# Performance work log

Hardware: AMD Instinct MI355X
Metric: run time of the kernel (lower is better)

Reference implementation:

```python
import jax, jax.numpy as jnp
import numpy as np

B, N_C, N_T = 8, 2048, 2048
D_S, D_F = 2, 1
K = 32
EMB_OBS = 4
H = 64
N_RBF = 16
NUM_BLKS = 6
RBF_GAMMA = 10.0


def _layer_norm(x, g, b):
    m = jnp.mean(x, -1, keepdims=True)
    v = jnp.var(x, -1, keepdims=True)
    return (x - m) * jax.lax.rsqrt(v + 1e-6) * g + b


def setup_inputs() -> dict:
    key = jax.random.key(0)
    ks = jax.random.split(key, 16)
    D_IN = EMB_OBS + D_S + D_F  # obs-flag embed + coords + features = 7
    return {
        "s_ctx": jax.random.normal(ks[0], (B, N_C, D_S)),
        "f_ctx": jax.random.normal(ks[1], (B, N_C, D_F)),
        "s_test": jax.random.normal(ks[2], (B, N_T, D_S)),
        "obs_table": jax.random.normal(ks[3], (2, EMB_OBS)) * 0.1,
        "emb_w0": jax.random.normal(ks[4], (D_IN, 256)) / np.sqrt(D_IN),
        "emb_b0": jnp.zeros((256,)),
        "emb_w1": jax.random.normal(ks[5], (256, 128)) / np.sqrt(256.0),
        "emb_b1": jnp.zeros((128,)),
        "emb_w2": jax.random.normal(ks[6], (128, H)) / np.sqrt(128.0),
        "emb_b2": jnp.zeros((H,)),
        "ln_g": jnp.ones((H,)),
        "ln_b": jnp.zeros((H,)),
        "rbf_centers": jnp.tile(jnp.linspace(0.0, 4.0, N_RBF)[None, :], (NUM_BLKS, 1)),
        "rbf_w": jax.random.normal(ks[7], (NUM_BLKS, N_RBF)) / np.sqrt(N_RBF),
        "rbf_b": jnp.zeros((NUM_BLKS,)),
        "blk_w1": jax.random.normal(ks[8], (NUM_BLKS, 2 * H, 2 * H)) / np.sqrt(2.0 * H),
        "blk_b1": jnp.zeros((NUM_BLKS, 2 * H)),
        "blk_w2": jax.random.normal(ks[9], (NUM_BLKS, 2 * H, H)) / np.sqrt(2.0 * H),
        "blk_b2": jnp.zeros((NUM_BLKS, H)),
        "blk_ln_g": jnp.ones((NUM_BLKS, H)),
        "blk_ln_b": jnp.zeros((NUM_BLKS, H)),
        "head_w0": jax.random.normal(ks[10], (H, 256)) / np.sqrt(float(H)),
        "head_b0": jnp.zeros((256,)),
        "head_w1": jax.random.normal(ks[11], (256, 64)) / np.sqrt(256.0),
        "head_b1": jnp.zeros((64,)),
        "head_w2": jax.random.normal(ks[12], (64, 2)) / np.sqrt(64.0),
        "head_b2": jnp.zeros((2,)),
    }


def reference(s_ctx, f_ctx, s_test, obs_table, emb_w0, emb_b0, emb_w1, emb_b1,
              emb_w2, emb_b2, ln_g, ln_b, rbf_centers, rbf_w, rbf_b,
              blk_w1, blk_b1, blk_w2, blk_b2, blk_ln_g, blk_ln_b,
              head_w0, head_b0, head_w1, head_b1, head_w2, head_b2):
    Bq, N_c = s_ctx.shape[:2]
    N_t = s_test.shape[1]

    # --- embed: obs flag + coords + (zeroed for test) function values ---
    obs_c = jnp.broadcast_to(obs_table[1], (Bq, N_c, EMB_OBS))  # observed = 1
    obs_t = jnp.broadcast_to(obs_table[0], (Bq, N_t, EMB_OBS))  # unobserved = 0
    f_test = jnp.zeros((Bq, N_t, f_ctx.shape[-1]), f_ctx.dtype)
    ctx = jnp.concatenate([obs_c, s_ctx, f_ctx], -1)
    test = jnp.concatenate([obs_t, s_test, f_test], -1)

    def emb(x):
        h = jax.nn.gelu(x @ emb_w0 + emb_b0)
        h = jax.nn.gelu(h @ emb_w1 + emb_b1)
        return h @ emb_w2 + emb_b2

    x_ctx = _layer_norm(emb(ctx), ln_g, ln_b)
    x_test = _layer_norm(emb(test), ln_g, ln_b)

    # --- kNN graph build (queries -> context senders) ---
    def knn(q, s):
        d2 = jnp.sum((q[:, :, None, :] - s[:, None, :, :]) ** 2, -1)  # (B, Nq, Nc)
        neg, idx = jax.lax.top_k(-d2, K)
        return idx, jnp.sqrt(jnp.maximum(-neg, 1e-12))

    idx_cc, d_cc = knn(s_ctx, s_ctx)
    idx_ct, d_ct = knn(s_test, s_ctx)
    off = (jnp.arange(Bq) * N_c)[:, None, None]
    senders = jnp.concatenate([(idx_cc + off).reshape(-1), (idx_ct + off).reshape(-1)])
    edges = jnp.concatenate([d_cc.reshape(-1), d_ct.reshape(-1)])
    nodes = jnp.concatenate([x_ctx.reshape(Bq * N_c, H), x_test.reshape(Bq * N_t, H)], 0)
    n_node = Bq * (N_c + N_t)
    # receivers = repeat(arange(n_node), K): each node owns a contiguous K-edge block
    send2d = senders.reshape(n_node, K)
    e2d = edges.reshape(n_node, K)
    mask2d = jnp.isfinite(e2d)
    e_safe = jnp.where(mask2d, e2d, 0.0)

    # --- RBF-biased message-passing blocks ---
    for l in range(NUM_BLKS):
        feats = jnp.exp(-RBF_GAMMA * (e_safe[..., None] - rbf_centers[l]) ** 2)  # (n_node, K, N_RBF)
        bias = feats @ rbf_w[l] + rbf_b[l]                                       # (n_node, K)
        bias = jnp.where(mask2d, bias, -1e9)
        w = jax.nn.softmax(bias, axis=-1)
        agg = jnp.einsum('nk,nkh->nh', w, nodes[send2d])  # gather senders + weighted sum
        h = jnp.concatenate([nodes, agg], -1)
        h = jax.nn.gelu(h @ blk_w1[l] + blk_b1[l])
        h = h @ blk_w2[l] + blk_b2[l]
        nodes = _layer_norm(nodes + h, blk_ln_g[l], blk_ln_b[l])

    # --- head + diagonal MVN ---
    x_t = nodes[-Bq * N_t:].reshape(Bq, N_t, H)
    h = jax.nn.gelu(x_t @ head_w0 + head_b0)
    h = jax.nn.gelu(h @ head_w1 + head_b1)
    out = h @ head_w2 + head_b2
    mean = out[..., 0]
    std = jax.nn.softplus(out[..., 1]) + 1e-3
    return mean, std
```

## Files before the change

kernel.cpp:

```cpp
#include <hip/hip_runtime.h>
#include <hip/hip_bf16.h>
#include <hip/hip_fp16.h>
#include <math.h>

using bf16 = __hip_bfloat16;

#define N_CTX   2048
#define N_TST   2048
#define NB      8
#define KNN     32
#define HDIM    64
#define NRBF    16
#define N_CTX_NODES (NB * N_CTX)
#define N_NODE      (NB * (N_CTX + N_TST))
#define POOL_CAP 256

typedef __attribute__((ext_vector_type(8))) short short8;
typedef __attribute__((ext_vector_type(4))) float f32x4;

#define SWZ(r, k) ((k) ^ (((r) & 7) << 3))

__device__ __forceinline__ bool is_f32(const void* probe) {
    return ((const unsigned short*)probe)[0] == 0;
}
__device__ __forceinline__ float ld(const void* p, int i, bool f32) {
    return f32 ? ((const float*)p)[i]
               : __bfloat162float(((const bf16*)p)[i]);
}
__device__ __forceinline__ unsigned short f2b(float x) {
    bf16 h = __float2bfloat16(x); unsigned short u;
    __builtin_memcpy(&u, &h, 2); return u;
}
__device__ __forceinline__ float b2f(unsigned short u) {
    bf16 h; __builtin_memcpy(&h, &u, 2); return __bfloat162float(h);
}
__device__ __forceinline__ unsigned short f2h(float x) {
    __half h = __float2half(x); unsigned short u;
    __builtin_memcpy(&u, &h, 2); return u;
}
__device__ __forceinline__ float h2f(unsigned short u) {
    __half h; __builtin_memcpy(&h, &u, 2); return __half2float(h);
}
__device__ __forceinline__ float gelu_tanh(float x) {
    float u = -1.5957691216057308f * (x + 0.044715f * x * x * x);
    return x * __builtin_amdgcn_rcpf(1.0f + __expf(u));
}
__device__ __forceinline__ unsigned long long shfl_u64(unsigned long long v, int src) {
    int lo = __shfl((int)(unsigned)v, src);
    int hi = __shfl((int)(unsigned)(v >> 32), src);
    return ((unsigned long long)(unsigned)hi << 32) | (unsigned)lo;
}

__device__ __forceinline__ void batch_barrier(unsigned* cnt, unsigned target) {
    __syncthreads();
    if (threadIdx.x == 0) {
        __hip_atomic_fetch_add(cnt, 1u, __ATOMIC_RELEASE, __HIP_MEMORY_SCOPE_AGENT);
        unsigned v;
        do {
            v = __hip_atomic_load(cnt, __ATOMIC_ACQUIRE, __HIP_MEMORY_SCOPE_AGENT);
            if (v < target) __builtin_amdgcn_s_sleep(2);
        } while (v < target);
    }
    __syncthreads();
}

__global__ __launch_bounds__(512)
void embed_kernel(const void* s_ctx, const void* f_ctx, const void* s_test,
                  const void* obs, const void* w0, const void* b0,
                  const void* w1, const void* b1, const void* w2, const void* b2,
                  const void* ln_g, const void* ln_b,
                  unsigned short* __restrict__ ctxb, float* __restrict__ testf) {
    bool f32 = is_f32(ln_g);
    int tid = threadIdx.x, w = tid >> 6, l = tid & 63;
    int nb = blockIdx.x * 64;
    bool is_test = (nb >= N_CTX_NODES);
    int loc0 = is_test ? nb - N_CTX_NODES : nb;
    int b = loc0 >> 11;

    __shared__ unsigned short A[64 * 128];
    __shared__ unsigned short W[256 * 128];
    __shared__ unsigned short H0[64 * 256];
    __shared__ unsigned short W2[64 * 128];

    for (int idx = tid; idx < 64 * 128; idx += 512) A[idx] = 0;
    for (int idx = tid; idx < 256 * 128; idx += 512) W[idx] = 0;
    __syncthreads();

    {
        int nn = tid >> 3, slot = tid & 7;
        if (slot < 7) {
            int loc = loc0 + nn;
            int i = loc & (N_CTX - 1);
            float v;
            if (slot < 4)       v = ld(obs, (is_test ? 0 : 1) * 4 + slot, f32);
            else if (slot < 6)  v = is_test ? ld(s_test, (b * N_TST + i) * 2 + slot - 4, f32)
                                            : ld(s_ctx,  (b * N_CTX + i) * 2 + slot - 4, f32);
            else                v = is_test ? 0.0f : ld(f_ctx, b * N_CTX + i, f32);
            A[nn * 128 + SWZ(nn, slot)] = f2b(v);
        }
    }
    for (int idx = tid; idx < 7 * 256; idx += 512) {
        int k = idx >> 8, c = idx & 255;
        W[c * 128 + SWZ(c, k)] = f2b(ld(w0, idx, f32));
    }
    __syncthreads();

    {
        int rt = w & 3, co = w >> 2;
        int ra = rt * 16 + (l & 15);
        int kb = (l >> 4) << 3;
        short8 av = *(const short8*)&A[ra * 128 + SWZ(ra, kb)];
        f32x4 acc[8];
        #pragma unroll
        for (int c8 = 0; c8 < 8; ++c8) acc[c8] = (f32x4){0.f, 0.f, 0.f, 0.f};
        #pragma unroll
        for (int c8 = 0; c8 < 8; ++c8) {
            int cb = co * 8 + c8;
            int rb = cb * 16 + (l & 15);
            short8 bv = *(const short8*)&W[rb * 128 + SWZ(rb, kb)];
            acc[c8] = __builtin_amdgcn_mfma_f32_16x16x32_bf16(av, bv, acc[c8], 0, 0, 0);
        }
        #pragma unroll
        for (int c8 = 0; c8 < 8; ++c8) {
            int col = (co * 8 + c8) * 16 + (l & 15);
            float bb = ld(b0, col, f32);
            #pragma unroll
            for (int reg = 0; reg < 4; ++reg) {
                int r = rt * 16 + (l >> 4) * 4 + reg;
                H0[r * 256 + SWZ(r, col)] = f2b(gelu_tanh(acc[c8][reg] + bb));
            }
        }
    }
    __syncthreads();

    for (int idx = tid; idx < 256 * 128; idx += 512) {
        int k = idx >> 7, c = idx & 127;
        W[c * 256 + SWZ(c, k)] = f2b(ld(w1, idx, f32));
    }
    for (int idx = tid; idx < 128 * 64; idx += 512) {
        int k = idx >> 6, c = idx & 63;
        W2[c * 128 + SWZ(c, k)] = f2b(ld(w2, idx, f32));
    }
    __syncthreads();

    {
        int rt = w & 3, cq = w >> 2;
        int ra = rt * 16 + (l & 15);
        f32x4 acc[4];
        #pragma unroll
        for (int c4 = 0; c4 < 4; ++c4) acc[c4] = (f32x4){0.f, 0.f, 0.f, 0.f};
        #pragma unroll
        for (int ks = 0; ks < 8; ++ks) {
            int kb = ks * 32 + ((l >> 4) << 3);
            short8 av = *(const short8*)&H0[ra * 256 + SWZ(ra, kb)];
            #pragma unroll
            for (int c4 = 0; c4 < 4; ++c4) {
                int cb = cq * 4 + c4;
                int rb = cb * 16 + (l & 15);
                short8 bv = *(const short8*)&W[rb * 256 + SWZ(rb, kb)];
                acc[c4] = __builtin_amdgcn_mfma_f32_16x16x32_bf16(av, bv, acc[c4], 0, 0, 0);
            }
        }
        #pragma unroll
        for (int c4 = 0; c4 < 4; ++c4) {
            int col = (cq * 4 + c4) * 16 + (l & 15);
            float bb = ld(b1, col, f32);
            #pragma unroll
            for (int reg = 0; reg < 4; ++reg) {
                int r = rt * 16 + (l >> 4) * 4 + reg;
                A[r * 128 + SWZ(r, col)] = f2b(gelu_tanh(acc[c4][reg] + bb));
            }
        }
    }
    __syncthreads();

    if (w < 4) {
        f32x4 a2[4];
        #pragma unroll
        for (int cb = 0; cb < 4; ++cb) a2[cb] = (f32x4){0.f, 0.f, 0.f, 0.f};
        int ra = w * 16 + (l & 15);
        #pragma unroll
        for (int ks = 0; ks < 4; ++ks) {
            int kb = ks * 32 + ((l >> 4) << 3);
            short8 av = *(const short8*)&A[ra * 128 + SWZ(ra, kb)];
            #pragma unroll
            for (int cb = 0; cb < 4; ++cb) {
                int rb = cb * 16 + (l & 15);
                short8 bv = *(const short8*)&W2[rb * 128 + SWZ(rb, kb)];
                a2[cb] = __builtin_amdgcn_mfma_f32_16x16x32_bf16(av, bv, a2[cb], 0, 0, 0);
            }
        }
        int colb = l & 15;
        float g4[4], bb4[4], b24[4];
        #pragma unroll
        for (int cb = 0; cb < 4; ++cb) {
            int col = cb * 16 + colb;
            g4[cb]  = ld(ln_g, col, f32);
            bb4[cb] = ld(ln_b, col, f32);
            b24[cb] = ld(b2,  col, f32);
        }
        #pragma unroll
        for (int reg = 0; reg < 4; ++reg) {
            int r = w * 16 + (l >> 4) * 4 + reg;
            float vv[4]; float s = 0.f, s2 = 0.f;
            #pragma unroll
            for (int cb = 0; cb < 4; ++cb) {
                float v = a2[cb][reg] + b24[cb];
                vv[cb] = v; s += v; s2 += v * v;
            }
            #pragma unroll
            for (int o = 8; o > 0; o >>= 1) { s += __shfl_xor(s, o); s2 += __shfl_xor(s2, o); }
            float m = s / 64.0f;
            float var = s2 / 64.0f - m * m;
            float rs = rsqrtf(var + 1e-6f);
            #pragma unroll
            for (int cb = 0; cb < 4; ++cb) {
                int col = cb * 16 + colb;
                float val = (vv[cb] - m) * rs * g4[cb] + bb4[cb];
                if (is_test) testf[(loc0 + r) * HDIM + col] = val;
                else         ctxb[(size_t)(nb + r) * HDIM + col] = f2b(val);
            }
        }
    }
}

__global__ __launch_bounds__(512) void knn_kernel(const void* s_ctx, const void* s_test,
                                                  const void* probe,
                                                  unsigned short* __restrict__ knn_idx) {
    bool f32 = is_f32(probe);
    int w = threadIdx.x >> 6, l = threadIdx.x & 63;
    int n = blockIdx.x * 8 + w;
    __shared__ float cx[N_CTX], cy[N_CTX];
    __shared__ unsigned long long pool[8][POOL_CAP];
    __shared__ unsigned pcnt[8];

    bool is_test = (n >= N_CTX_NODES);
    int loc = is_test ? n - N_CTX_NODES : n;
    int b = loc >> 11, q = loc & (N_CTX - 1);

    for (int j = threadIdx.x; j < N_CTX; j += 512) {
        cx[j] = ld(s_ctx, (b * N_CTX + j) * 2 + 0, f32);
        cy[j] = ld(s_ctx, (b * N_CTX + j) * 2 + 1, f32);
    }
    __syncthreads();

    float qx = is_test ? ld(s_test, (b * N_TST + q) * 2 + 0, f32) : cx[q];
    float qy = is_test ? ld(s_test, (b * N_TST + q) * 2 + 1, f32) : cy[q];

    unsigned dbits[32];
    unsigned bmin = 0xFFFFFFFFu;
    #pragma unroll
    for (int i = 0; i < 32; ++i) {
        int j = i * 64 + l;
        float dx = qx - cx[j], dy = qy - cy[j];
        float d2 = __fadd_rn(__fmul_rn(dx, dx), __fmul_rn(dy, dy));
        unsigned ub = __float_as_uint(d2);
        dbits[i] = ub;
        bmin = min(bmin, ub);
    }

    unsigned T = 0;
    #pragma unroll
    for (int bit = 31; bit >= 0; --bit) {
        unsigned trial = T | (1u << bit);
        int c = __popcll(__ballot(bmin < trial));
        if (c < 32) T = trial;
    }

    if (l == 0) pcnt[w] = 0;
    unsigned mycnt = 0;
    #pragma unroll
    for (int i = 0; i < 32; ++i) mycnt += (dbits[i] <= T) ? 1u : 0u;
    unsigned off = atomicAdd(&pcnt[w], mycnt);
    #pragma unroll
    for (int i = 0; i < 32; ++i) {
        if (dbits[i] <= T) {
            if (off < POOL_CAP)
                pool[w][off] = ((unsigned long long)dbits[i] << 32) | (unsigned)(i * 64 + l);
            ++off;
        }
    }
    asm volatile("s_waitcnt lgkmcnt(0)" ::: "memory");
    unsigned M = pcnt[w];
    if (M > POOL_CAP) M = POOL_CAP;

    if (M <= 128) {
        unsigned long long my0 = (l < (int)M) ? pool[w][l] : ~0ull;
        unsigned long long my1 = (64 + l < (int)M) ? pool[w][64 + l] : ~0ull;
        unsigned r0 = 0, r1 = 0;
        unsigned M0 = M < 64 ? M : 64;
        for (unsigned jp = 0; jp < M0; ++jp) {
            unsigned long long v = shfl_u64(my0, (int)jp);
            r0 += (v < my0) ? 1u : 0u;
            r1 += (v < my1) ? 1u : 0u;
        }
        for (unsigned jp = 64; jp < M; ++jp) {
            unsigned long long v = shfl_u64(my1, (int)(jp - 64));
            r0 += (v < my0) ? 1u : 0u;
            r1 += (v < my1) ? 1u : 0u;
        }
        if (l < (int)M && r0 < KNN)
            knn_idx[(size_t)n * KNN + r0] = (unsigned short)(my0 & 0xFFFFu);
        if (64 + l < (int)M && r1 < KNN)
            knn_idx[(size_t)n * KNN + r1] = (unsigned short)(my1 & 0xFFFFu);
    } else {
        for (unsigned m = l; m < M; m += 64) {
            unsigned long long me = pool[w][m];
            unsigned rank = 0;
            for (unsigned jp = 0; jp < M; ++jp)
                rank += (pool[w][jp] < me) ? 1u : 0u;
            if (rank < KNN)
                knn_idx[(size_t)n * KNN + rank] = (unsigned short)(me & 0xFFFFu);
        }
    }
}

__global__ __launch_bounds__(1024, 4)
void mp_coop_kernel(unsigned short* __restrict__ ctxA, unsigned short* __restrict__ ctxB,
                    float* __restrict__ testf,
                    const unsigned short* __restrict__ kidx,
                    unsigned* __restrict__ bar,
                    const void* s_ctx, const void* s_test,
                    const void* rbf_c, const void* rbf_w, const void* rbf_b,
                    const void* w1, const void* b1, const void* w2, const void* b2,
                    const void* lng, const void* lnb) {
    bool f32 = is_f32(lng);
    int tid = threadIdx.x, w = tid >> 6, l = tid & 63;

    int batch = blockIdx.x & 7;
    int slot  = blockIdx.x >> 3;
    bool isctx = (slot < 16);
    int lslot = slot & 15;
    int seg0 = batch * N_CTX + lslot * 128;
    int n0   = (isctx ? 0 : N_CTX_NODES) + seg0;
    int bofs = batch * N_CTX;
    unsigned* cnt = bar + batch * 16;

    __shared__ float          state[128 * 64];
    __shared__ unsigned short A0[128 * 128];
    __shared__ unsigned short h1s[128 * 128];
    __shared__ unsigned short wt[128 * 128];
    __shared__ unsigned short wk_l[128 * 32];
    __shared__ unsigned short kidx_l[128 * 32];
    __shared__ unsigned short d_l[128 * 32];

    for (int idx = tid; idx < 128 * 64; idx += 1024)
        state[idx] = isctx ? b2f(ctxA[n0 * 64 + idx]) : testf[seg0 * 64 + idx];

    for (int idx = tid; idx < 4096; idx += 1024) {
        int i = idx >> 5, kk = idx & 31;
        int n = n0 + i;
        int q = lslot * 128 + i;
        float qx = isctx ? ld(s_ctx, (bofs + q) * 2 + 0, f32)
                         : ld(s_test, (batch * N_TST + q) * 2 + 0, f32);
        float qy = isctx ? ld(s_ctx, (bofs + q) * 2 + 1, f32)
                         : ld(s_test, (batch * N_TST + q) * 2 + 1, f32);
        int si = (int)kidx[(size_t)n * KNN + kk];
        kidx_l[idx] = (unsigned short)si;
        float dx = qx - ld(s_ctx, (bofs + si) * 2 + 0, f32);
        float dy = qy - ld(s_ctx, (bofs + si) * 2 + 1, f32);
        float d2 = __fadd_rn(__fmul_rn(dx, dx), __fmul_rn(dy, dy));
        d_l[idx] = f2h(sqrtf(fmaxf(d2, 1e-12f)));
    }
    __syncthreads();

    const unsigned short* cur = ctxA;
    unsigned short* nxt = ctxB;

    for (int layer = 0; layer < 6; ++layer) {
        for (int idx = tid; idx < 16384; idx += 1024) {
            int k = idx >> 7, c = idx & 127;
            wt[c * 128 + SWZ(c, k)] = f2b(ld(w1, layer * 16384 + idx, f32));
        }
        for (int p = 0; p < 4; ++p) {
            int i = p * 32 + w * 2 + (l >> 5);
            int kk = l & 31;
            float d = h2f(d_l[i * 32 + kk]);
            float bias = ld(rbf_b, layer, f32);
            #pragma unroll
            for (int j = 0; j < NRBF; ++j) {
                float c = ld(rbf_c, layer * NRBF + j, f32);
                float u = d - c;
                bias += expf(-10.0f * u * u) * ld(rbf_w, layer * NRBF + j, f32);
            }
            float m = bias;
            #pragma unroll
            for (int o = 16; o > 0; o >>= 1) m = fmaxf(m, __shfl_xor(m, o));
            float e = expf(bias - m), s = e;
            #pragma unroll
            for (int o = 16; o > 0; o >>= 1) s += __shfl_xor(s, o);
            wk_l[i * 32 + kk] = f2h(e / s);
        }
        __syncthreads();

        {
            int m = l & 31, h = l >> 5;
            for (int i = w * 8; i < w * 8 + 8; ++i) {
                A0[i * 128 + SWZ(i, l)] = f2b(state[i * 64 + l]);
                float a0 = 0.f, a1 = 0.f, c0 = 0.f, c1 = 0.f;
                #pragma unroll
                for (int k = 0; k < 16; k += 2) {
                    {
                        int kk = 2 * k + h;
                        int si = (int)kidx_l[i * 32 + kk];
                        unsigned u = *(const unsigned*)(cur + (size_t)(bofs + si) * 64 + 2 * m);
                        float wkv = h2f(wk_l[i * 32 + kk]);
                        a0 += wkv * __uint_as_float(u << 16);
                        a1 += wkv * __uint_as_float(u & 0xFFFF0000u);
                    }
                    {
                        int kk = 2 * (k + 1) + h;
                        int si = (int)kidx_l[i * 32 + kk];
                        unsigned u = *(const unsigned*)(cur + (size_t)(bofs + si) * 64 + 2 * m);
                        float wkv = h2f(wk_l[i * 32 + kk]);
                        c0 += wkv * __uint_as_float(u << 16);
                        c1 += wkv * __uint_as_float(u & 0xFFFF0000u);
                    }
                }
                a0 += c0; a1 += c1;
                a0 += __shfl_xor(a0, 32);
                a1 += __shfl_xor(a1, 32);
                if (h == 0) {
                    unsigned pk = (unsigned)f2b(a0) | ((unsigned)f2b(a1) << 16);
                    *(unsigned*)&A0[i * 128 + SWZ(i, 64 + 2 * m)] = pk;
                }
            }
        }
        __syncthreads();

        {
            f32x4 acc[4];
            #pragma unroll
            for (int c4 = 0; c4 < 4; ++c4) acc[c4] = (f32x4){0.f, 0.f, 0.f, 0.f};
            int ra = (w & 7) * 16 + (l & 15);
            #pragma unroll
            for (int ks = 0; ks < 4; ++ks) {
                int kb = ks * 32 + ((l >> 4) << 3);
                short8 av = *(const short8*)&A0[ra * 128 + SWZ(ra, kb)];
                #pragma unroll
                for (int c4 = 0; c4 < 4; ++c4) {
                    int cb = (w >> 3) * 4 + c4;
                    int rb = cb * 16 + (l & 15);
                    short8 bv = *(const short8*)&wt[rb * 128 + SWZ(rb, kb)];
                    acc[c4] = __builtin_amdgcn_mfma_f32_16x16x32_bf16(av, bv, acc[c4], 0, 0, 0);
                }
            }
            #pragma unroll
            for (int c4 = 0; c4 < 4; ++c4) {
                int col = ((w >> 3) * 4 + c4) * 16 + (l & 15);
                float bb = ld(b1, layer * 128 + col, f32);
                #pragma unroll
                for (int reg = 0; reg < 4; ++reg) {
                    int r = (w & 7) * 16 + (l >> 4) * 4 + reg;
                    h1s[r * 128 + SWZ(r, col)] = f2b(gelu_tanh(acc[c4][reg] + bb));
                }
            }
        }
        __syncthreads();
        for (int idx = tid; idx < 8192; idx += 1024) {
            int k = idx >> 6, c = idx & 63;
            wt[c * 128 + SWZ(c, k)] = f2b(ld(w2, layer * 8192 + idx, f32));
        }
        __syncthreads();

        if (w < 8) {
            f32x4 a2[4];
            #pragma unroll
            for (int cb = 0; cb < 4; ++cb) a2[cb] = (f32x4){0.f, 0.f, 0.f, 0.f};
            int ra = w * 16 + (l & 15);
            #pragma unroll
            for (int ks = 0; ks < 4; ++ks) {
                int kb = ks * 32 + ((l >> 4) << 3);
                short8 av = *(const short8*)&h1s[ra * 128 + SWZ(ra, kb)];
                #pragma unroll
                for (int cb = 0; cb < 4; ++cb) {
                    int rb = cb * 16 + (l & 15);
                    short8 bv = *(const short8*)&wt[rb * 128 + SWZ(rb, kb)];
                    a2[cb] = __builtin_amdgcn_mfma_f32_16x16x32_bf16(av, bv, a2[cb], 0, 0, 0);
                }
            }
            int colb = l & 15;
            float g4[4], bb4[4], b24[4];
            #pragma unroll
            for (int cb = 0; cb < 4; ++cb) {
                int col = cb * 16 + colb;
                g4[cb]  = ld(lng, layer * 64 + col, f32);
                bb4[cb] = ld(lnb, layer * 64 + col, f32);
                b24[cb] = ld(b2,  layer * 64 + col, f32);
            }
            #pragma unroll
            for (int reg = 0; reg < 4; ++reg) {
                int r = w * 16 + (l >> 4) * 4 + reg;
                float vv[4]; float s = 0.f, s2 = 0.f;
                #pragma unroll
                for (int cb = 0; cb < 4; ++cb) {
                    int col = cb * 16 + colb;
                    float v = a2[cb][reg] + b24[cb] + state[r * 64 + col];
                    vv[cb] = v; s += v; s2 += v * v;
                }
                #pragma unroll
                for (int o = 8; o > 0; o >>= 1) { s += __shfl_xor(s, o); s2 += __shfl_xor(s2, o); }
                float m = s / 64.0f;
                float var = s2 / 64.0f - m * m;
                float rs = rsqrtf(var + 1e-6f);
                #pragma unroll
                for (int cb = 0; cb < 4; ++cb) {
                    int col = cb * 16 + colb;
                    state[r * 64 + col] = (vv[cb] - m) * rs * g4[cb] + bb4[cb];
                }
            }
        }
        __syncthreads();

        if (layer < 5) {
            if (isctx)
                for (int idx = tid; idx < 128 * 64; idx += 1024)
                    nxt[n0 * 64 + idx] = f2b(state[idx]);
            batch_barrier(cnt, 32u * (unsigned)(layer + 1));
            const unsigned short* t1 = cur; cur = nxt; nxt = (unsigned short*)t1;
        }
    }

    if (!isctx)
        for (int idx = tid; idx < 128 * 64; idx += 1024)
            testf[seg0 * 64 + idx] = state[idx];
}

__global__ void head_kernel(const float* __restrict__ testf,
                            const void* w0, const void* b0, const void* w1, const void* b1,
                            const void* w2, const void* b2, const void* probe, void* out) {
    bool f32 = is_f32(probe);
    int t = threadIdx.x;
    int pb = blockIdx.x * 8;
    __shared__ float xs[8][64];
    __shared__ float h0[8][256];
    __shared__ float h1[8][64];

    xs[t >> 6][t & 63] = testf[(pb + (t >> 6)) * HDIM + (t & 63)];
    { int i1 = t + 256; xs[i1 >> 6][i1 & 63] = testf[(pb + (i1 >> 6)) * HDIM + (i1 & 63)]; }
    __syncthreads();

    {
        float bb = ld(b0, t, f32);
        float a[8];
        #pragma unroll
        for (int j = 0; j < 8; ++j) a[j] = bb;
        for (int i = 0; i < 64; ++i) {
            float wv = ld(w0, i * 256 + t, f32);
            #pragma unroll
            for (int j = 0; j < 8; ++j) a[j] += xs[j][i] * wv;
        }
        #pragma unroll
        for (int j = 0; j < 8; ++j) h0[j][t] = gelu_tanh(a[j]);
    }
    __syncthreads();

    {
        int c = t & 63, g = t >> 6;
        float bb = ld(b1, c, f32);
        float a0 = bb, a1 = bb;
        for (int i = 0; i < 256; ++i) {
            float wv = ld(w1, i * 64 + c, f32);
            a0 += h0[g][i] * wv;
            a1 += h0[g + 4][i] * wv;
        }
        h1[g][c]     = gelu_tanh(a0);
        h1[g + 4][c] = gelu_tanh(a1);
    }
    __syncthreads();

    if (t < 16) {
        int nn = t >> 1, j = t & 1;
        float a = ld(b2, j, f32);
        for (int i = 0; i < 64; ++i) a += h1[nn][i] * ld(w2, i * 2 + j, f32);
        float r;
        if (j == 0) r = a;
        else        r = fmaxf(a, 0.0f) + log1pf(expf(-fabsf(a))) + 1e-3f;
        int oi = j * 16384 + pb + nn;
        if (f32) ((float*)out)[oi] = r;
        else     ((bf16*)out)[oi]  = __float2bfloat16(r);
    }
}

extern "C" void kernel_launch(void* const* d_in, const int* in_sizes, int n_in,
                              void* d_out, int out_size, void* d_ws, size_t ws_size,
                              hipStream_t stream) {
    void* s_ctx   = d_in[0];
    void* f_ctx   = d_in[1];
    void* s_test  = d_in[2];
    void* obs     = d_in[3];
    void* emb_w0  = d_in[4];
    void* emb_b0  = d_in[5];
    void* emb_w1  = d_in[6];
    void* emb_b1  = d_in[7];
    void* emb_w2  = d_in[8];
    void* emb_b2  = d_in[9];
    void* ln_g    = d_in[10];
    void* ln_b    = d_in[11];
    void* rbf_c   = d_in[12];
    void* rbf_w   = d_in[13];
    void* rbf_b   = d_in[14];
    void* blk_w1  = d_in[15];
    void* blk_b1  = d_in[16];
    void* blk_w2  = d_in[17];
    void* blk_b2  = d_in[18];
    void* blk_lng = d_in[19];
    void* blk_lnb = d_in[20];
    void* head_w0 = d_in[21];
    void* head_b0 = d_in[22];
    void* head_w1 = d_in[23];
    void* head_b1 = d_in[24];
    void* head_w2 = d_in[25];
    void* head_b2 = d_in[26];

    unsigned short* ctxA  = (unsigned short*)d_ws;
    unsigned short* ctxB  = (unsigned short*)((char*)d_ws + 2097152);
    float*          testf = (float*)((char*)d_ws + 4194304);
    unsigned short* kidx  = (unsigned short*)((char*)d_ws + 8388608);
    unsigned*       bar   = (unsigned*)((char*)d_ws + 10485760);

    hipMemsetAsync(bar, 0, 8 * 16 * sizeof(unsigned), stream);

    embed_kernel<<<N_NODE / 64, 512, 0, stream>>>(s_ctx, f_ctx, s_test, obs,
        emb_w0, emb_b0, emb_w1, emb_b1, emb_w2, emb_b2, ln_g, ln_b, ctxA, testf);

    knn_kernel<<<N_NODE / 8, 512, 0, stream>>>(s_ctx, s_test, ln_g, kidx);

    void* kargs[] = { &ctxA, &ctxB, &testf, &kidx, &bar, &s_ctx, &s_test,
                      &rbf_c, &rbf_w, &rbf_b,
                      &blk_w1, &blk_b1, &blk_w2, &blk_b2, &blk_lng, &blk_lnb };
    hipLaunchCooperativeKernel((void*)mp_coop_kernel, dim3(256), dim3(1024),
                               kargs, 0, stream);

    head_kernel<<<16384 / 8, 256, 0, stream>>>(testf,
        head_w0, head_b0, head_w1, head_b1, head_w2, head_b2, ln_g, d_out);
}
```

Measured before the change: 446.6 us.

## Template kernels on dtype, batch gather loads, double head rows per block

Each kernel body becomes a template on the input dtype, so the per-load runtime f32/bf16 branch is resolved at compile time. The neighbour gather in the message-passing loop now issues eight independent loads before accumulating, to expose more memory-level parallelism. The head kernel handles 16 test points per block instead of 8, halving the block count and reusing each weight load across more rows, at the cost of more registers and shared memory per block.

```diff
diff --git a/kernel.cpp b/kernel.cpp
--- a/kernel.cpp
+++ b/kernel.cpp
@@ -23,6 +23,11 @@
 __device__ __forceinline__ bool is_f32(const void* probe) {
     return ((const unsigned short*)probe)[0] == 0;
 }
+template<bool F32>
+__device__ __forceinline__ float ldT(const void* p, int i) {
+    if constexpr (F32) return ((const float*)p)[i];
+    else               return __bfloat162float(((const bf16*)p)[i]);
+}
 __device__ __forceinline__ float ld(const void* p, int i, bool f32) {
     return f32 ? ((const float*)p)[i]
                : __bfloat162float(((const bf16*)p)[i]);
@@ -64,164 +69,176 @@
     __syncthreads();
 }
 
+template<bool F32>
+__device__ __forceinline__ void embed_body(
+        const void* s_ctx, const void* f_ctx, const void* s_test, const void* obs,
+        const void* w0, const void* b0, const void* w1, const void* b1,
+        const void* w2, const void* b2, const void* ln_g, const void* ln_b,
+        unsigned short* __restrict__ ctxb, float* __restrict__ testf,
+        unsigned short* A, unsigned short* W, unsigned short* H0, unsigned short* W2) {
+    int tid = threadIdx.x, w = tid >> 6, l = tid & 63;
+    int nb = blockIdx.x * 64;
+    bool is_test = (nb >= N_CTX_NODES);
+    int loc0 = is_test ? nb - N_CTX_NODES : nb;
+    int b = loc0 >> 11;
+
+    for (int idx = tid; idx < 64 * 128; idx += 512) A[idx] = 0;
+    for (int idx = tid; idx < 256 * 128; idx += 512) W[idx] = 0;
+    __syncthreads();
+
+    {   int nn = tid >> 3, slot = tid & 7;
+        if (slot < 7) {
+            int loc = loc0 + nn;
+            int i = loc & (N_CTX - 1);
+            float v;
+            if (slot < 4)       v = ldT<F32>(obs, (is_test ? 0 : 1) * 4 + slot);
+            else if (slot < 6)  v = is_test ? ldT<F32>(s_test, (b * N_TST + i) * 2 + slot - 4)
+                                            : ldT<F32>(s_ctx,  (b * N_CTX + i) * 2 + slot - 4);
+            else                v = is_test ? 0.0f : ldT<F32>(f_ctx, b * N_CTX + i);
+            A[nn * 128 + SWZ(nn, slot)] = f2b(v);
+        }
+    }
+    for (int idx = tid; idx < 7 * 256; idx += 512) {
+        int k = idx >> 8, c = idx & 255;
+        W[c * 128 + SWZ(c, k)] = f2b(ldT<F32>(w0, idx));
+    }
+    __syncthreads();
+
+    {
+        int rt = w & 3, co = w >> 2;
+        int ra = rt * 16 + (l & 15);
+        int kb = (l >> 4) << 3;
+        short8 av = *(const short8*)&A[ra * 128 + SWZ(ra, kb)];
+        f32x4 acc[8];
+        #pragma unroll
+        for (int c8 = 0; c8 < 8; ++c8) acc[c8] = (f32x4){0.f, 0.f, 0.f, 0.f};
+        #pragma unroll
+        for (int c8 = 0; c8 < 8; ++c8) {
+            int cb = co * 8 + c8;
+            int rb = cb * 16 + (l & 15);
+            short8 bv = *(const short8*)&W[rb * 128 + SWZ(rb, kb)];
+            acc[c8] = __builtin_amdgcn_mfma_f32_16x16x32_bf16(av, bv, acc[c8], 0, 0, 0);
+        }
+        #pragma unroll
+        for (int c8 = 0; c8 < 8; ++c8) {
+            int col = (co * 8 + c8) * 16 + (l & 15);
+            float bb = ldT<F32>(b0, col);
+            #pragma unroll
+            for (int reg = 0; reg < 4; ++reg) {
+                int r = rt * 16 + (l >> 4) * 4 + reg;
+                H0[r * 256 + SWZ(r, col)] = f2b(gelu_tanh(acc[c8][reg] + bb));
+            }
+        }
+    }
+    __syncthreads();
+
+    for (int idx = tid; idx < 256 * 128; idx += 512) {
+        int k = idx >> 7, c = idx & 127;
+        W[c * 256 + SWZ(c, k)] = f2b(ldT<F32>(w1, idx));
+    }
+    for (int idx = tid; idx < 128 * 64; idx += 512) {
+        int k = idx >> 6, c = idx & 63;
+        W2[c * 128 + SWZ(c, k)] = f2b(ldT<F32>(w2, idx));
+    }
+    __syncthreads();
+
+    {
+        int rt = w & 3, cq = w >> 2;
+        int ra = rt * 16 + (l & 15);
+        f32x4 acc[4];
+        #pragma unroll
+        for (int c4 = 0; c4 < 4; ++c4) acc[c4] = (f32x4){0.f, 0.f, 0.f, 0.f};
+        #pragma unroll
+        for (int ks = 0; ks < 8; ++ks) {
+            int kb = ks * 32 + ((l >> 4) << 3);
+            short8 av = *(const short8*)&H0[ra * 256 + SWZ(ra, kb)];
+            #pragma unroll
+            for (int c4 = 0; c4 < 4; ++c4) {
+                int cb = cq * 4 + c4;
+                int rb = cb * 16 + (l & 15);
+                short8 bv = *(const short8*)&W[rb * 256 + SWZ(rb, kb)];
+                acc[c4] = __builtin_amdgcn_mfma_f32_16x16x32_bf16(av, bv, acc[c4], 0, 0, 0);
+            }
+        }
+        #pragma unroll
+        for (int c4 = 0; c4 < 4; ++c4) {
+            int col = (cq * 4 + c4) * 16 + (l & 15);
+            float bb = ldT<F32>(b1, col);
+            #pragma unroll
+            for (int reg = 0; reg < 4; ++reg) {
+                int r = rt * 16 + (l >> 4) * 4 + reg;
+                A[r * 128 + SWZ(r, col)] = f2b(gelu_tanh(acc[c4][reg] + bb));
+            }
+        }
+    }
+    __syncthreads();
+
+    if (w < 4) {
+        f32x4 a2[4];
+        #pragma unroll
+        for (int cb = 0; cb < 4; ++cb) a2[cb] = (f32x4){0.f, 0.f, 0.f, 0.f};
+        int ra = w * 16 + (l & 15);
+        #pragma unroll
+        for (int ks = 0; ks < 4; ++ks) {
+            int kb = ks * 32 + ((l >> 4) << 3);
+            short8 av = *(const short8*)&A[ra * 128 + SWZ(ra, kb)];
+            #pragma unroll
+            for (int cb = 0; cb < 4; ++cb) {
+                int rb = cb * 16 + (l & 15);
+                short8 bv = *(const short8*)&W2[rb * 128 + SWZ(rb, kb)];
+                a2[cb] = __builtin_amdgcn_mfma_f32_16x16x32_bf16(av, bv, a2[cb], 0, 0, 0);
+            }
+        }
+        int colb = l & 15;
+        float g4[4], bb4[4], b24[4];
+        #pragma unroll
+        for (int cb = 0; cb < 4; ++cb) {
+            int col = cb * 16 + colb;
+            g4[cb]  = ldT<F32>(ln_g, col);
+            bb4[cb] = ldT<F32>(ln_b, col);
+            b24[cb] = ldT<F32>(b2,  col);
+        }
+        #pragma unroll
+        for (int reg = 0; reg < 4; ++reg) {
+            int r = w * 16 + (l >> 4) * 4 + reg;
+            float vv[4]; float s = 0.f, s2 = 0.f;
+            #pragma unroll
+            for (int cb = 0; cb < 4; ++cb) {
+                float v = a2[cb][reg] + b24[cb];
+                vv[cb] = v; s += v; s2 += v * v;
+            }
+            #pragma unroll
+            for (int o = 8; o > 0; o >>= 1) { s += __shfl_xor(s, o); s2 += __shfl_xor(s2, o); }
+            float m = s / 64.0f;
+            float var = s2 / 64.0f - m * m;
+            float rs = rsqrtf(var + 1e-6f);
+            #pragma unroll
+            for (int cb = 0; cb < 4; ++cb) {
+                int col = cb * 16 + colb;
+                float val = (vv[cb] - m) * rs * g4[cb] + bb4[cb];
+                if (is_test) testf[(loc0 + r) * HDIM + col] = val;
+                else         ctxb[(size_t)(nb + r) * HDIM + col] = f2b(val);
+            }
+        }
+    }
+}
+
 __global__ __launch_bounds__(512)
 void embed_kernel(const void* s_ctx, const void* f_ctx, const void* s_test,
                   const void* obs, const void* w0, const void* b0,
                   const void* w1, const void* b1, const void* w2, const void* b2,
                   const void* ln_g, const void* ln_b,
                   unsigned short* __restrict__ ctxb, float* __restrict__ testf) {
-    bool f32 = is_f32(ln_g);
-    int tid = threadIdx.x, w = tid >> 6, l = tid & 63;
-    int nb = blockIdx.x * 64;
-    bool is_test = (nb >= N_CTX_NODES);
-    int loc0 = is_test ? nb - N_CTX_NODES : nb;
-    int b = loc0 >> 11;
-
     __shared__ unsigned short A[64 * 128];
     __shared__ unsigned short W[256 * 128];
     __shared__ unsigned short H0[64 * 256];
     __shared__ unsigned short W2[64 * 128];
-
-    for (int idx = tid; idx < 64 * 128; idx += 512) A[idx] = 0;
-    for (int idx = tid; idx < 256 * 128; idx += 512) W[idx] = 0;
-    __syncthreads();
-
-    {
-        int nn = tid >> 3, slot = tid & 7;
-        if (slot < 7) {
-            int loc = loc0 + nn;
-            int i = loc & (N_CTX - 1);
-            float v;
-            if (slot < 4)       v = ld(obs, (is_test ? 0 : 1) * 4 + slot, f32);
-            else if (slot < 6)  v = is_test ? ld(s_test, (b * N_TST + i) * 2 + slot - 4, f32)
-                                            : ld(s_ctx,  (b * N_CTX + i) * 2 + slot - 4, f32);
-            else                v = is_test ? 0.0f : ld(f_ctx, b * N_CTX + i, f32);
-            A[nn * 128 + SWZ(nn, slot)] = f2b(v);
-        }
-    }
-    for (int idx = tid; idx < 7 * 256; idx += 512) {
-        int k = idx >> 8, c = idx & 255;
-        W[c * 128 + SWZ(c, k)] = f2b(ld(w0, idx, f32));
-    }
-    __syncthreads();
-
-    {
-        int rt = w & 3, co = w >> 2;
-        int ra = rt * 16 + (l & 15);
-        int kb = (l >> 4) << 3;
-        short8 av = *(const short8*)&A[ra * 128 + SWZ(ra, kb)];
-        f32x4 acc[8];
-        #pragma unroll
-        for (int c8 = 0; c8 < 8; ++c8) acc[c8] = (f32x4){0.f, 0.f, 0.f, 0.f};
-        #pragma unroll
-        for (int c8 = 0; c8 < 8; ++c8) {
-            int cb = co * 8 + c8;
-            int rb = cb * 16 + (l & 15);
-            short8 bv = *(const short8*)&W[rb * 128 + SWZ(rb, kb)];
-            acc[c8] = __builtin_amdgcn_mfma_f32_16x16x32_bf16(av, bv, acc[c8], 0, 0, 0);
-        }
-        #pragma unroll
-        for (int c8 = 0; c8 < 8; ++c8) {
-            int col = (co * 8 + c8) * 16 + (l & 15);
-            float bb = ld(b0, col, f32);
-            #pragma unroll
-            for (int reg = 0; reg < 4; ++reg) {
-                int r = rt * 16 + (l >> 4) * 4 + reg;
-                H0[r * 256 + SWZ(r, col)] = f2b(gelu_tanh(acc[c8][reg] + bb));
-            }
-        }
-    }
-    __syncthreads();
-
-    for (int idx = tid; idx < 256 * 128; idx += 512) {
-        int k = idx >> 7, c = idx & 127;
-        W[c * 256 + SWZ(c, k)] = f2b(ld(w1, idx, f32));
-    }
-    for (int idx = tid; idx < 128 * 64; idx += 512) {
-        int k = idx >> 6, c = idx & 63;
-        W2[c * 128 + SWZ(c, k)] = f2b(ld(w2, idx, f32));
-    }
-    __syncthreads();
-
-    {
-        int rt = w & 3, cq = w >> 2;
-        int ra = rt * 16 + (l & 15);
-        f32x4 acc[4];
-        #pragma unroll
-        for (int c4 = 0; c4 < 4; ++c4) acc[c4] = (f32x4){0.f, 0.f, 0.f, 0.f};
-        #pragma unroll
-        for (int ks = 0; ks < 8; ++ks) {
-            int kb = ks * 32 + ((l >> 4) << 3);
-            short8 av = *(const short8*)&H0[ra * 256 + SWZ(ra, kb)];
-            #pragma unroll
-            for (int c4 = 0; c4 < 4; ++c4) {
-                int cb = cq * 4 + c4;
-                int rb = cb * 16 + (l & 15);
-                short8 bv = *(const short8*)&W[rb * 256 + SWZ(rb, kb)];
-                acc[c4] = __builtin_amdgcn_mfma_f32_16x16x32_bf16(av, bv, acc[c4], 0, 0, 0);
-            }
-        }
-        #pragma unroll
-        for (int c4 = 0; c4 < 4; ++c4) {
-            int col = (cq * 4 + c4) * 16 + (l & 15);
-            float bb = ld(b1, col, f32);
-            #pragma unroll
-            for (int reg = 0; reg < 4; ++reg) {
-                int r = rt * 16 + (l >> 4) * 4 + reg;
-                A[r * 128 + SWZ(r, col)] = f2b(gelu_tanh(acc[c4][reg] + bb));
-            }
-        }
-    }
-    __syncthreads();
-
-    if (w < 4) {
-        f32x4 a2[4];
-        #pragma unroll
-        for (int cb = 0; cb < 4; ++cb) a2[cb] = (f32x4){0.f, 0.f, 0.f, 0.f};
-        int ra = w * 16 + (l & 15);
-        #pragma unroll
-        for (int ks = 0; ks < 4; ++ks) {
-            int kb = ks * 32 + ((l >> 4) << 3);
-            short8 av = *(const short8*)&A[ra * 128 + SWZ(ra, kb)];
-            #pragma unroll
-            for (int cb = 0; cb < 4; ++cb) {
-                int rb = cb * 16 + (l & 15);
-                short8 bv = *(const short8*)&W2[rb * 128 + SWZ(rb, kb)];
-                a2[cb] = __builtin_amdgcn_mfma_f32_16x16x32_bf16(av, bv, a2[cb], 0, 0, 0);
-            }
-        }
-        int colb = l & 15;
-        float g4[4], bb4[4], b24[4];
-        #pragma unroll
-        for (int cb = 0; cb < 4; ++cb) {
-            int col = cb * 16 + colb;
-            g4[cb]  = ld(ln_g, col, f32);
-            bb4[cb] = ld(ln_b, col, f32);
-            b24[cb] = ld(b2,  col, f32);
-        }
-        #pragma unroll
-        for (int reg = 0; reg < 4; ++reg) {
-            int r = w * 16 + (l >> 4) * 4 + reg;
-            float vv[4]; float s = 0.f, s2 = 0.f;
-            #pragma unroll
-            for (int cb = 0; cb < 4; ++cb) {
-                float v = a2[cb][reg] + b24[cb];
-                vv[cb] = v; s += v; s2 += v * v;
-            }
-            #pragma unroll
-            for (int o = 8; o > 0; o >>= 1) { s += __shfl_xor(s, o); s2 += __shfl_xor(s2, o); }
-            float m = s / 64.0f;
-            float var = s2 / 64.0f - m * m;
-            float rs = rsqrtf(var + 1e-6f);
-            #pragma unroll
-            for (int cb = 0; cb < 4; ++cb) {
-                int col = cb * 16 + colb;
-                float val = (vv[cb] - m) * rs * g4[cb] + bb4[cb];
-                if (is_test) testf[(loc0 + r) * HDIM + col] = val;
-                else         ctxb[(size_t)(nb + r) * HDIM + col] = f2b(val);
-            }
-        }
-    }
+    if (is_f32(ln_g))
+        embed_body<true>(s_ctx, f_ctx, s_test, obs, w0, b0, w1, b1, w2, b2,
+                         ln_g, ln_b, ctxb, testf, A, W, H0, W2);
+    else
+        embed_body<false>(s_ctx, f_ctx, s_test, obs, w0, b0, w1, b1, w2, b2,
+                          ln_g, ln_b, ctxb, testf, A, W, H0, W2);
 }
 
 __global__ __launch_bounds__(512) void knn_kernel(const void* s_ctx, const void* s_test,
@@ -315,16 +332,16 @@
     }
 }
 
-__global__ __launch_bounds__(1024, 4)
-void mp_coop_kernel(unsigned short* __restrict__ ctxA, unsigned short* __restrict__ ctxB,
-                    float* __restrict__ testf,
-                    const unsigned short* __restrict__ kidx,
-                    unsigned* __restrict__ bar,
-                    const void* s_ctx, const void* s_test,
-                    const void* rbf_c, const void* rbf_w, const void* rbf_b,
-                    const void* w1, const void* b1, const void* w2, const void* b2,
-                    const void* lng, const void* lnb) {
-    bool f32 = is_f32(lng);
+template<bool F32>
+__device__ __forceinline__ void mp_body(
+        unsigned short* __restrict__ ctxA, unsigned short* __restrict__ ctxB,
+        float* __restrict__ testf, const unsigned short* __restrict__ kidx,
+        unsigned* __restrict__ bar, const void* s_ctx, const void* s_test,
+        const void* rbf_c, const void* rbf_w, const void* rbf_b,
+        const void* w1, const void* b1, const void* w2, const void* b2,
+        const void* lng, const void* lnb,
+        float* state, unsigned short* A0, unsigned short* h1s, unsigned short* wt,
+        unsigned short* wk_l, unsigned short* kidx_l, unsigned short* d_l) {
     int tid = threadIdx.x, w = tid >> 6, l = tid & 63;
 
     int batch = blockIdx.x & 7;
@@ -336,14 +353,6 @@
     int bofs = batch * N_CTX;
     unsigned* cnt = bar + batch * 16;
 
-    __shared__ float          state[128 * 64];
-    __shared__ unsigned short A0[128 * 128];
-    __shared__ unsigned short h1s[128 * 128];
-    __shared__ unsigned short wt[128 * 128];
-    __shared__ unsigned short wk_l[128 * 32];
-    __shared__ unsigned short kidx_l[128 * 32];
-    __shared__ unsigned short d_l[128 * 32];
-
     for (int idx = tid; idx < 128 * 64; idx += 1024)
         state[idx] = isctx ? b2f(ctxA[n0 * 64 + idx]) : testf[seg0 * 64 + idx];
 
@@ -351,14 +360,14 @@
         int i = idx >> 5, kk = idx & 31;
         int n = n0 + i;
         int q = lslot * 128 + i;
-        float qx = isctx ? ld(s_ctx, (bofs + q) * 2 + 0, f32)
-                         : ld(s_test, (batch * N_TST + q) * 2 + 0, f32);
-        float qy = isctx ? ld(s_ctx, (bofs + q) * 2 + 1, f32)
-                         : ld(s_test, (batch * N_TST + q) * 2 + 1, f32);
+        float qx = isctx ? ldT<F32>(s_ctx, (bofs + q) * 2 + 0)
+                         : ldT<F32>(s_test, (batch * N_TST + q) * 2 + 0);
+        float qy = isctx ? ldT<F32>(s_ctx, (bofs + q) * 2 + 1)
+                         : ldT<F32>(s_test, (batch * N_TST + q) * 2 + 1);
         int si = (int)kidx[(size_t)n * KNN + kk];
         kidx_l[idx] = (unsigned short)si;
-        float dx = qx - ld(s_ctx, (bofs + si) * 2 + 0, f32);
-        float dy = qy - ld(s_ctx, (bofs + si) * 2 + 1, f32);
+        float dx = qx - ldT<F32>(s_ctx, (bofs + si) * 2 + 0);
+        float dy = qy - ldT<F32>(s_ctx, (bofs + si) * 2 + 1);
         float d2 = __fadd_rn(__fmul_rn(dx, dx), __fmul_rn(dy, dy));
         d_l[idx] = f2h(sqrtf(fmaxf(d2, 1e-12f)));
     }
@@ -370,18 +379,18 @@
     for (int layer = 0; layer < 6; ++layer) {
         for (int idx = tid; idx < 16384; idx += 1024) {
             int k = idx >> 7, c = idx & 127;
-            wt[c * 128 + SWZ(c, k)] = f2b(ld(w1, layer * 16384 + idx, f32));
+            wt[c * 128 + SWZ(c, k)] = f2b(ldT<F32>(w1, layer * 16384 + idx));
         }
         for (int p = 0; p < 4; ++p) {
             int i = p * 32 + w * 2 + (l >> 5);
             int kk = l & 31;
             float d = h2f(d_l[i * 32 + kk]);
-            float bias = ld(rbf_b, layer, f32);
+            float bias = ldT<F32>(rbf_b, layer);
             #pragma unroll
             for (int j = 0; j < NRBF; ++j) {
-                float c = ld(rbf_c, layer * NRBF + j, f32);
+                float c = ldT<F32>(rbf_c, layer * NRBF + j);
                 float u = d - c;
-                bias += expf(-10.0f * u * u) * ld(rbf_w, layer * NRBF + j, f32);
+                bias += expf(-10.0f * u * u) * ldT<F32>(rbf_w, layer * NRBF + j);
             }
             float m = bias;
             #pragma unroll
@@ -395,29 +404,26 @@
 
         {
             int m = l & 31, h = l >> 5;
+            const char* cbase = (const char*)cur + 4 * m + (size_t)bofs * 128;
             for (int i = w * 8; i < w * 8 + 8; ++i) {
                 A0[i * 128 + SWZ(i, l)] = f2b(state[i * 64 + l]);
-                float a0 = 0.f, a1 = 0.f, c0 = 0.f, c1 = 0.f;
+                float a0 = 0.f, a1 = 0.f;
                 #pragma unroll
-                for (int k = 0; k < 16; k += 2) {
-                    {
-                        int kk = 2 * k + h;
-                        int si = (int)kidx_l[i * 32 + kk];
-                        unsigned u = *(const unsigned*)(cur + (size_t)(bofs + si) * 64 + 2 * m);
-                        float wkv = h2f(wk_l[i * 32 + kk]);
-                        a0 += wkv * __uint_as_float(u << 16);
-                        a1 += wkv * __uint_as_float(u & 0xFFFF0000u);
+                for (int half = 0; half < 2; ++half) {
+                    unsigned uu[8]; float wv[8];
+                    #pragma unroll
+                    for (int j = 0; j < 8; ++j) {
+                        int kk = 2 * (8 * half + j) + h;
+                        unsigned off = ((unsigned)kidx_l[i * 32 + kk]) << 7;
+                        uu[j] = *(const unsigned*)(cbase + off);
+                        wv[j] = h2f(wk_l[i * 32 + kk]);
                     }
-                    {
-                        int kk = 2 * (k + 1) + h;
-                        int si = (int)kidx_l[i * 32 + kk];
-                        unsigned u = *(const unsigned*)(cur + (size_t)(bofs + si) * 64 + 2 * m);
-                        float wkv = h2f(wk_l[i * 32 + kk]);
-                        c0 += wkv * __uint_as_float(u << 16);
-                        c1 += wkv * __uint_as_float(u & 0xFFFF0000u);
+                    #pragma unroll
+                    for (int j = 0; j < 8; ++j) {
+                        a0 += wv[j] * __uint_as_float(uu[j] << 16);
+                        a1 += wv[j] * __uint_as_float(uu[j] & 0xFFFF0000u);
                     }
                 }
-                a0 += c0; a1 += c1;
                 a0 += __shfl_xor(a0, 32);
                 a1 += __shfl_xor(a1, 32);
                 if (h == 0) {
@@ -448,7 +454,7 @@
             #pragma unroll
             for (int c4 = 0; c4 < 4; ++c4) {
                 int col = ((w >> 3) * 4 + c4) * 16 + (l & 15);
-                float bb = ld(b1, layer * 128 + col, f32);
+                float bb = ldT<F32>(b1, layer * 128 + col);
                 #pragma unroll
                 for (int reg = 0; reg < 4; ++reg) {
                     int r = (w & 7) * 16 + (l >> 4) * 4 + reg;
@@ -459,7 +465,7 @@
         __syncthreads();
         for (int idx = tid; idx < 8192; idx += 1024) {
             int k = idx >> 6, c = idx & 63;
-            wt[c * 128 + SWZ(c, k)] = f2b(ld(w2, layer * 8192 + idx, f32));
+            wt[c * 128 + SWZ(c, k)] = f2b(ldT<F32>(w2, layer * 8192 + idx));
         }
         __syncthreads();
 
@@ -484,9 +490,9 @@
             #pragma unroll
             for (int cb = 0; cb < 4; ++cb) {
                 int col = cb * 16 + colb;
-                g4[cb]  = ld(lng, layer * 64 + col, f32);
-                bb4[cb] = ld(lnb, layer * 64 + col, f32);
-                b24[cb] = ld(b2,  layer * 64 + col, f32);
+                g4[cb]  = ldT<F32>(lng, layer * 64 + col);
+                bb4[cb] = ldT<F32>(lnb, layer * 64 + col);
+                b24[cb] = ldT<F32>(b2,  layer * 64 + col);
             }
             #pragma unroll
             for (int reg = 0; reg < 4; ++reg) {
@@ -526,60 +532,92 @@
             testf[seg0 * 64 + idx] = state[idx];
 }
 
-__global__ void head_kernel(const float* __restrict__ testf,
-                            const void* w0, const void* b0, const void* w1, const void* b1,
-                            const void* w2, const void* b2, const void* probe, void* out) {
-    bool f32 = is_f32(probe);
+__global__ __launch_bounds__(1024, 4)
+void mp_coop_kernel(unsigned short* __restrict__ ctxA, unsigned short* __restrict__ ctxB,
+                    float* __restrict__ testf,
+                    const unsigned short* __restrict__ kidx,
+                    unsigned* __restrict__ bar,
+                    const void* s_ctx, const void* s_test,
+                    const void* rbf_c, const void* rbf_w, const void* rbf_b,
+                    const void* w1, const void* b1, const void* w2, const void* b2,
+                    const void* lng, const void* lnb) {
+    __shared__ float          state[128 * 64];
+    __shared__ unsigned short A0[128 * 128];
+    __shared__ unsigned short h1s[128 * 128];
+    __shared__ unsigned short wt[128 * 128];
+    __shared__ unsigned short wk_l[128 * 32];
+    __shared__ unsigned short kidx_l[128 * 32];
+    __shared__ unsigned short d_l[128 * 32];
+    if (is_f32(lng))
+        mp_body<true>(ctxA, ctxB, testf, kidx, bar, s_ctx, s_test, rbf_c, rbf_w, rbf_b,
+                      w1, b1, w2, b2, lng, lnb, state, A0, h1s, wt, wk_l, kidx_l, d_l);
+    else
+        mp_body<false>(ctxA, ctxB, testf, kidx, bar, s_ctx, s_test, rbf_c, rbf_w, rbf_b,
+                       w1, b1, w2, b2, lng, lnb, state, A0, h1s, wt, wk_l, kidx_l, d_l);
+}
+
+template<bool F32>
+__device__ __forceinline__ void head_body(
+        const float* __restrict__ testf, const void* w0, const void* b0,
+        const void* w1, const void* b1, const void* w2, const void* b2, void* out,
+        float (*xs)[64], float (*h0)[256], float (*h1)[64]) {
     int t = threadIdx.x;
-    int pb = blockIdx.x * 8;
-    __shared__ float xs[8][64];
-    __shared__ float h0[8][256];
-    __shared__ float h1[8][64];
-
-    xs[t >> 6][t & 63] = testf[(pb + (t >> 6)) * HDIM + (t & 63)];
-    { int i1 = t + 256; xs[i1 >> 6][i1 & 63] = testf[(pb + (i1 >> 6)) * HDIM + (i1 & 63)]; }
+    int pb = blockIdx.x * 16;
+
+    for (int idx = t; idx < 1024; idx += 256)
+        xs[idx >> 6][idx & 63] = testf[(pb + (idx >> 6)) * HDIM + (idx & 63)];
     __syncthreads();
 
     {
-        float bb = ld(b0, t, f32);
-        float a[8];
-        #pragma unroll
-        for (int j = 0; j < 8; ++j) a[j] = bb;
+        float bb = ldT<F32>(b0, t);
+        float a[16];
+        #pragma unroll
+        for (int j = 0; j < 16; ++j) a[j] = bb;
         for (int i = 0; i < 64; ++i) {
-            float wv = ld(w0, i * 256 + t, f32);
-            #pragma unroll
-            for (int j = 0; j < 8; ++j) a[j] += xs[j][i] * wv;
-        }
-        #pragma unroll
-        for (int j = 0; j < 8; ++j) h0[j][t] = gelu_tanh(a[j]);
+            float wv = ldT<F32>(w0, i * 256 + t);
+            #pragma unroll
+            for (int j = 0; j < 16; ++j) a[j] += xs[j][i] * wv;
+        }
+        #pragma unroll
+        for (int j = 0; j < 16; ++j) h0[j][t] = gelu_tanh(a[j]);
     }
     __syncthreads();
 
     {
         int c = t & 63, g = t >> 6;
-        float bb = ld(b1, c, f32);
-        float a0 = bb, a1 = bb;
+        float bb = ldT<F32>(b1, c);
+        float a0 = bb, a1 = bb, a2 = bb, a3 = bb;
         for (int i = 0; i < 256; ++i) {
-            float wv = ld(w1, i * 64 + c, f32);
-            a0 += h0[g][i] * wv;
-            a1 += h0[g + 4][i] * wv;
-        }
-        h1[g][c]     = gelu_tanh(a0);
-        h1[g + 4][c] = gelu_tanh(a1);
-    }
-    __syncthreads();
-
-    if (t < 16) {
+            float wv = ldT<F32>(w1, i * 64 + c);
+            a0 += h0[g][i] * wv;      a1 += h0[g + 4][i] * wv;
+            a2 += h0[g + 8][i] * wv;  a3 += h0[g + 12][i] * wv;
+        }
+        h1[g][c]      = gelu_tanh(a0); h1[g + 4][c]  = gelu_tanh(a1);
+        h1[g + 8][c]  = gelu_tanh(a2); h1[g + 12][c] = gelu_tanh(a3);
+    }
+    __syncthreads();
+
+    if (t < 32) {
         int nn = t >> 1, j = t & 1;
-        float a = ld(b2, j, f32);
-        for (int i = 0; i < 64; ++i) a += h1[nn][i] * ld(w2, i * 2 + j, f32);
+        float a = ldT<F32>(b2, j);
+        for (int i = 0; i < 64; ++i) a += h1[nn][i] * ldT<F32>(w2, i * 2 + j);
         float r;
         if (j == 0) r = a;
         else        r = fmaxf(a, 0.0f) + log1pf(expf(-fabsf(a))) + 1e-3f;
         int oi = j * 16384 + pb + nn;
-        if (f32) ((float*)out)[oi] = r;
-        else     ((bf16*)out)[oi]  = __float2bfloat16(r);
-    }
+        if constexpr (F32) ((float*)out)[oi] = r;
+        else               ((bf16*)out)[oi]  = __float2bfloat16(r);
+    }
+}
+
+__global__ void head_kernel(const float* __restrict__ testf,
+                            const void* w0, const void* b0, const void* w1, const void* b1,
+                            const void* w2, const void* b2, const void* probe, void* out) {
+    __shared__ float xs[16][64];
+    __shared__ float h0[16][256];
+    __shared__ float h1[16][64];
+    if (is_f32(probe)) head_body<true>(testf, w0, b0, w1, b1, w2, b2, out, xs, h0, h1);
+    else               head_body<false>(testf, w0, b0, w1, b1, w2, b2, out, xs, h0, h1);
 }
 
 extern "C" void kernel_launch(void* const* d_in, const int* in_sizes, int n_in,
@@ -632,6 +670,6 @@
     hipLaunchCooperativeKernel((void*)mp_coop_kernel, dim3(256), dim3(1024),
                                kargs, 0, stream);
 
-    head_kernel<<<16384 / 8, 256, 0, stream>>>(testf,
+    head_kernel<<<16384 / 16, 256, 0, stream>>>(testf,
         head_w0, head_b0, head_w1, head_b1, head_w2, head_b2, ln_g, d_out);
 }
```

Result: slower. 456.7 us (+2.2%).
